# Optimization experiments

Hardware: AMD Instinct MI355X
Metric: run time of the kernel (lower is better)

The kernel has to match this reference:

```python
import jax, jax.numpy as jnp
import numpy as np

VOCAB = 8
HIDDEN = 768
DINUC_DIM = HIDDEN // 4  # 192
LN_EPS = 1e-12


def _dinuc_ids(input_ids):
    # nucleotide_map = {4:0,5:1,6:2,7:3}; dinuc id = first*4 + second if both valid else 0
    a = input_ids[:, :-1]
    b = input_ids[:, 1:]
    valid = (a >= 4) & (a <= 7) & (b >= 4) & (b <= 7)
    ids = (a - 4) * 4 + (b - 4)
    return jnp.where(valid, ids, 0)


def setup_inputs() -> dict:
    key = jax.random.key(0)
    ks = jax.random.split(key, 7)
    B, S = 32, 2048
    input_ids = jax.random.randint(ks[0], (B, S), 0, VOCAB, dtype=jnp.int64)
    token_emb = jax.random.normal(ks[1], (VOCAB, HIDDEN), dtype=jnp.float32) * 0.02
    dinuc_emb = jax.random.normal(ks[2], (16, DINUC_DIM), dtype=jnp.float32) * 0.02
    proj_W = jax.random.normal(ks[3], (HIDDEN, HIDDEN + DINUC_DIM), dtype=jnp.float32) * 0.02  # [out, in] torch layout
    proj_b = jax.random.normal(ks[4], (HIDDEN,), dtype=jnp.float32) * 0.02
    ln_gamma = jnp.ones((HIDDEN,), dtype=jnp.float32)
    ln_beta = jnp.zeros((HIDDEN,), dtype=jnp.float32)
    return {"input_ids": input_ids, "token_emb": token_emb, "dinuc_emb": dinuc_emb,
            "proj_W": proj_W, "proj_b": proj_b, "ln_gamma": ln_gamma, "ln_beta": ln_beta}


def reference(input_ids, token_emb, dinuc_emb, proj_W, proj_b, ln_gamma, ln_beta):
    # token embedding lookup: [B,S,H]
    embeddings = token_emb[input_ids]
    # dinucleotide embedding, padded with one zero row at the end: [B,S,H/4]
    d_ids = _dinuc_ids(input_ids)                      # [B,S-1]
    d_emb = dinuc_emb[d_ids]                           # [B,S-1,H/4]
    d_emb = jnp.pad(d_emb, ((0, 0), (0, 1), (0, 0)))   # [B,S,H/4]
    # concat + linear projection back to H
    concat = jnp.concatenate([embeddings, d_emb], axis=-1)  # [B,S,H+H/4]
    x = jnp.einsum('bsi,oi->bso', concat, proj_W) + proj_b
    # layernorm (eps=1e-12), dropout is identity in eval
    mu = jnp.mean(x, axis=-1, keepdims=True)
    var = jnp.mean((x - mu) ** 2, axis=-1, keepdims=True)
    return (x - mu) / jnp.sqrt(var + LN_EPS) * ln_gamma + ln_beta
```

## Files before the change

kernel.cpp:

```cpp
#include <hip/hip_runtime.h>

#define VOCAB   8
#define HIDDEN  768
#define DINUC   192
#define CONCAT  960
#define NDID    17
#define NROWS   (VOCAB * NDID)
#define SEQ     2048
#define BATCH   32
#define LN_EPS  1e-12f

__global__ void k_td(const float* __restrict__ tok,
                     const float* __restrict__ din,
                     const float* __restrict__ W,
                     float* __restrict__ TD) {
    int t = blockIdx.x * blockDim.x + threadIdx.x;
    if (t >= 24 * HIDDEN) return;
    int r = t / HIDDEN;
    int o = t - r * HIDDEN;

    float acc = 0.f;
    if (r < VOCAB) {
        const float4* e = (const float4*)(tok + r * HIDDEN);
        const float4* w = (const float4*)(W + (size_t)o * CONCAT);
        #pragma unroll 4
        for (int i = 0; i < HIDDEN / 4; ++i) {
            float4 ev = e[i], wv = w[i];
            acc += ev.x * wv.x + ev.y * wv.y + ev.z * wv.z + ev.w * wv.w;
        }
    } else {
        const float4* e = (const float4*)(din + (r - VOCAB) * DINUC);
        const float4* w = (const float4*)(W + (size_t)o * CONCAT + HIDDEN);
        #pragma unroll 4
        for (int i = 0; i < DINUC / 4; ++i) {
            float4 ev = e[i], wv = w[i];
            acc += ev.x * wv.x + ev.y * wv.y + ev.z * wv.z + ev.w * wv.w;
        }
    }
    TD[t] = acc;
}

__device__ inline float block_reduce_sum(float s, float* red) {
    int lane = threadIdx.x & 63;
    int wave = threadIdx.x >> 6;
    #pragma unroll
    for (int off = 32; off > 0; off >>= 1) s += __shfl_down(s, off, 64);
    if (lane == 0) red[wave] = s;
    __syncthreads();
    float tot = red[0] + red[1] + red[2] + red[3];
    __syncthreads();
    return tot;
}

__global__ void k_table(const float* __restrict__ TD,
                        const float* __restrict__ bias,
                        const float* __restrict__ gamma,
                        const float* __restrict__ beta,
                        float* __restrict__ table) {
    int row = blockIdx.x;
    int id  = row / NDID;
    int did = row - id * NDID;
    const float* T = TD + id * HIDDEN;
    const float* D = TD + (VOCAB + did) * HIDDEN;
    bool hasd = (did < 16);

    __shared__ float red[4];
    int tid = threadIdx.x;

    float v[3];
    float s = 0.f;
    #pragma unroll
    for (int k = 0; k < 3; ++k) {
        int o = tid + k * 256;
        float x = T[o] + bias[o];
        if (hasd) x += D[o];
        v[k] = x;
        s += x;
    }
    float mu = block_reduce_sum(s, red) * (1.f / HIDDEN);

    float sq = 0.f;
    #pragma unroll
    for (int k = 0; k < 3; ++k) {
        float d = v[k] - mu;
        sq += d * d;
    }
    float var = block_reduce_sum(sq, red) * (1.f / HIDDEN);
    float rstd = rsqrtf(var + LN_EPS);

    #pragma unroll
    for (int k = 0; k < 3; ++k) {
        int o = tid + k * 256;
        table[row * HIDDEN + o] = (v[k] - mu) * rstd * gamma[o] + beta[o];
    }
}

__global__ void k_bcast(const int* __restrict__ ids,
                        const float* __restrict__ table,
                        float4* __restrict__ out) {
    int row = blockIdx.x * 4 + threadIdx.y;
    int s   = row & (SEQ - 1);
    int a   = ids[row];
    int did;
    if (s == SEQ - 1) {
        did = 16;
    } else {
        int b = ids[row + 1];
        bool valid = (a >= 4) & (a <= 7) & (b >= 4) & (b <= 7);
        did = valid ? ((a - 4) * 4 + (b - 4)) : 0;
    }
    const float4* src = (const float4*)(table + (a * NDID + did) * HIDDEN);
    out[(size_t)row * (HIDDEN / 4) + threadIdx.x] = src[threadIdx.x];
}

extern "C" void kernel_launch(void* const* d_in, const int* in_sizes, int n_in,
                              void* d_out, int out_size, void* d_ws, size_t ws_size,
                              hipStream_t stream) {
    const int*   ids   = (const int*)d_in[0];
    const float* tok   = (const float*)d_in[1];
    const float* din   = (const float*)d_in[2];
    const float* W     = (const float*)d_in[3];
    const float* bias  = (const float*)d_in[4];
    const float* gamma = (const float*)d_in[5];
    const float* beta  = (const float*)d_in[6];

    float* table = (float*)d_ws;
    float* TD    = table + NROWS * HIDDEN;

    k_td   <<<(24 * HIDDEN + 255) / 256, 256, 0, stream>>>(tok, din, W, TD);
    k_table<<<NROWS, 256, 0, stream>>>(TD, bias, gamma, beta, table);
    k_bcast<<<(BATCH * SEQ) / 4, dim3(192, 4), 0, stream>>>(ids, table, (float4*)d_out);
}
```

Before: 265.4 us.

## Fuse projection matvec into LN table kernel and use nontemporal output stores

Drops the separate k_td kernel. Each of the 136 table-row blocks now computes the full 960-wide projection for its (token, dinuc) pair with wave-per-output dot products and shuffle reductions, then applies LayerNorm. This removes one launch and the TD round trip, but every block re-reads the whole W matrix (about 2.9 MB), so it does far more redundant work and W traffic than before. The broadcast kernel also switches to nontemporal stores for the 200 MB output to reduce cache pollution.

Measured after the change: 367.5 us. 38.4% more time.

```diff
diff --git a/kernel.cpp b/kernel.cpp
--- a/kernel.cpp
+++ b/kernel.cpp
@@ -10,74 +10,71 @@
 #define BATCH   32
 #define LN_EPS  1e-12f
 
-__global__ void k_td(const float* __restrict__ tok,
-                     const float* __restrict__ din,
-                     const float* __restrict__ W,
-                     float* __restrict__ TD) {
-    int t = blockIdx.x * blockDim.x + threadIdx.x;
-    if (t >= 24 * HIDDEN) return;
-    int r = t / HIDDEN;
-    int o = t - r * HIDDEN;
+typedef float v4f __attribute__((ext_vector_type(4)));
 
-    float acc = 0.f;
-    if (r < VOCAB) {
-        const float4* e = (const float4*)(tok + r * HIDDEN);
-        const float4* w = (const float4*)(W + (size_t)o * CONCAT);
-        #pragma unroll 4
-        for (int i = 0; i < HIDDEN / 4; ++i) {
-            float4 ev = e[i], wv = w[i];
-            acc += ev.x * wv.x + ev.y * wv.y + ev.z * wv.z + ev.w * wv.w;
-        }
-    } else {
-        const float4* e = (const float4*)(din + (r - VOCAB) * DINUC);
-        const float4* w = (const float4*)(W + (size_t)o * CONCAT + HIDDEN);
-        #pragma unroll 4
-        for (int i = 0; i < DINUC / 4; ++i) {
-            float4 ev = e[i], wv = w[i];
-            acc += ev.x * wv.x + ev.y * wv.y + ev.z * wv.z + ev.w * wv.w;
-        }
-    }
-    TD[t] = acc;
-}
-
-__device__ inline float block_reduce_sum(float s, float* red) {
-    int lane = threadIdx.x & 63;
-    int wave = threadIdx.x >> 6;
-    #pragma unroll
-    for (int off = 32; off > 0; off >>= 1) s += __shfl_down(s, off, 64);
-    if (lane == 0) red[wave] = s;
-    __syncthreads();
-    float tot = red[0] + red[1] + red[2] + red[3];
-    __syncthreads();
-    return tot;
-}
-
-__global__ void k_table(const float* __restrict__ TD,
-                        const float* __restrict__ bias,
-                        const float* __restrict__ gamma,
-                        const float* __restrict__ beta,
-                        float* __restrict__ table) {
+__global__ __launch_bounds__(256) void k_table(
+    const float* __restrict__ tok, const float* __restrict__ din,
+    const float* __restrict__ W, const float* __restrict__ bias,
+    const float* __restrict__ gamma, const float* __restrict__ beta,
+    float* __restrict__ table) {
     int row = blockIdx.x;
     int id  = row / NDID;
     int did = row - id * NDID;
-    const float* T = TD + id * HIDDEN;
-    const float* D = TD + (VOCAB + did) * HIDDEN;
-    bool hasd = (did < 16);
 
+    __shared__ float e[CONCAT];
+    __shared__ float x[HIDDEN];
     __shared__ float red[4];
+
     int tid = threadIdx.x;
+
+    for (int i = tid; i < HIDDEN; i += 256) e[i] = tok[id * HIDDEN + i];
+    if (tid < DINUC) e[HIDDEN + tid] = (did < 16) ? din[did * DINUC + tid] : 0.f;
+    __syncthreads();
+
+    int wave = tid >> 6;
+    int lane = tid & 63;
+    const float4* e4 = (const float4*)e;
+    float4 er0 = e4[lane];
+    float4 er1 = e4[64 + lane];
+    float4 er2 = e4[128 + lane];
+    float4 er3 = (lane < 48) ? e4[192 + lane] : make_float4(0.f, 0.f, 0.f, 0.f);
+
+    #pragma unroll 2
+    for (int i = 0; i < HIDDEN / 4; ++i) {
+        int o = wave * (HIDDEN / 4) + i;
+        const float4* w4 = (const float4*)(W + (size_t)o * CONCAT);
+        float4 a0 = w4[lane];
+        float4 a1 = w4[64 + lane];
+        float4 a2 = w4[128 + lane];
+        float4 a3 = (lane < 48) ? w4[192 + lane] : make_float4(0.f, 0.f, 0.f, 0.f);
+        float acc = er0.x * a0.x + er0.y * a0.y + er0.z * a0.z + er0.w * a0.w
+                  + er1.x * a1.x + er1.y * a1.y + er1.z * a1.z + er1.w * a1.w
+                  + er2.x * a2.x + er2.y * a2.y + er2.z * a2.z + er2.w * a2.w
+                  + er3.x * a3.x + er3.y * a3.y + er3.z * a3.z + er3.w * a3.w;
+        #pragma unroll
+        for (int m = 32; m; m >>= 1) acc += __shfl_xor(acc, m, 64);
+        if (lane == 0) x[o] = acc;
+    }
+    __syncthreads();
 
     float v[3];
     float s = 0.f;
     #pragma unroll
     for (int k = 0; k < 3; ++k) {
         int o = tid + k * 256;
-        float x = T[o] + bias[o];
-        if (hasd) x += D[o];
-        v[k] = x;
-        s += x;
+        float t = x[o] + bias[o];
+        v[k] = t;
+        s += t;
     }
-    float mu = block_reduce_sum(s, red) * (1.f / HIDDEN);
+    {
+        #pragma unroll
+        for (int off = 32; off; off >>= 1) s += __shfl_down(s, off, 64);
+        if (lane == 0) red[wave] = s;
+        __syncthreads();
+        s = red[0] + red[1] + red[2] + red[3];
+        __syncthreads();
+    }
+    float mu = s * (1.f / HIDDEN);
 
     float sq = 0.f;
     #pragma unroll
@@ -85,8 +82,15 @@
         float d = v[k] - mu;
         sq += d * d;
     }
-    float var = block_reduce_sum(sq, red) * (1.f / HIDDEN);
-    float rstd = rsqrtf(var + LN_EPS);
+    {
+        #pragma unroll
+        for (int off = 32; off; off >>= 1) sq += __shfl_down(sq, off, 64);
+        if (lane == 0) red[wave] = sq;
+        __syncthreads();
+        sq = red[0] + red[1] + red[2] + red[3];
+        __syncthreads();
+    }
+    float rstd = rsqrtf(sq * (1.f / HIDDEN) + LN_EPS);
 
     #pragma unroll
     for (int k = 0; k < 3; ++k) {
@@ -95,9 +99,10 @@
     }
 }
 
-__global__ void k_bcast(const int* __restrict__ ids,
-                        const float* __restrict__ table,
-                        float4* __restrict__ out) {
+__global__ __launch_bounds__(768) void k_bcast(
+    const int* __restrict__ ids,
+    const float* __restrict__ table,
+    v4f* __restrict__ out) {
     int row = blockIdx.x * 4 + threadIdx.y;
     int s   = row & (SEQ - 1);
     int a   = ids[row];
@@ -109,8 +114,9 @@
         bool valid = (a >= 4) & (a <= 7) & (b >= 4) & (b <= 7);
         did = valid ? ((a - 4) * 4 + (b - 4)) : 0;
     }
-    const float4* src = (const float4*)(table + (a * NDID + did) * HIDDEN);
-    out[(size_t)row * (HIDDEN / 4) + threadIdx.x] = src[threadIdx.x];
+    const v4f* src = (const v4f*)(table + (a * NDID + did) * HIDDEN);
+    v4f val = src[threadIdx.x];
+    __builtin_nontemporal_store(val, &out[(size_t)row * (HIDDEN / 4) + threadIdx.x]);
 }
 
 extern "C" void kernel_launch(void* const* d_in, const int* in_sizes, int n_in,
@@ -125,9 +131,7 @@
     const float* beta  = (const float*)d_in[6];
 
     float* table = (float*)d_ws;
-    float* TD    = table + NROWS * HIDDEN;
 
-    k_td   <<<(24 * HIDDEN + 255) / 256, 256, 0, stream>>>(tok, din, W, TD);
-    k_table<<<NROWS, 256, 0, stream>>>(TD, bias, gamma, beta, table);
-    k_bcast<<<(BATCH * SEQ) / 4, dim3(192, 4), 0, stream>>>(ids, table, (float4*)d_out);
+    k_table<<<NROWS, 256, 0, stream>>>(tok, din, W, bias, gamma, beta, table);
+    k_bcast<<<(BATCH * SEQ) / 4, dim3(192, 4), 0, stream>>>(ids, table, (v4f*)d_out);
 }
```

## Use wave-per-output dot products in k_td and nontemporal stores in broadcast

Applied to the files above, without the earlier changes.

The precompute kernel now assigns one 64-lane wave per output element. Lanes read contiguous float4 slices of the weight row and reduce with xor shuffles, replacing the old scheme where each thread looped serially over a full row with strided, uncoalesced weight reads. The broadcast kernel writes its roughly 200 MB output with nontemporal stores to avoid polluting the cache, and launch bounds are added to all three kernels. The main cost targeted is bandwidth on the output writes plus the serial latency of the small GEMV.

New measurement: 240.6 us. 9.4% less time.

```diff
diff --git a/kernel.cpp b/kernel.cpp
--- a/kernel.cpp
+++ b/kernel.cpp
@@ -10,41 +10,45 @@
 #define BATCH   32
 #define LN_EPS  1e-12f
 
-__global__ void k_td(const float* __restrict__ tok,
-                     const float* __restrict__ din,
-                     const float* __restrict__ W,
-                     float* __restrict__ TD) {
-    int t = blockIdx.x * blockDim.x + threadIdx.x;
-    if (t >= 24 * HIDDEN) return;
-    int r = t / HIDDEN;
-    int o = t - r * HIDDEN;
+typedef float v4f __attribute__((ext_vector_type(4)));
+
+__global__ __launch_bounds__(256) void k_td(
+    const float* __restrict__ tok, const float* __restrict__ din,
+    const float* __restrict__ W, float* __restrict__ TD) {
+    int w    = (blockIdx.x * 256 + threadIdx.x) >> 6;
+    int lane = threadIdx.x & 63;
+    int r    = w / HIDDEN;
+    int o    = w - r * HIDDEN;
 
     float acc = 0.f;
     if (r < VOCAB) {
-        const float4* e = (const float4*)(tok + r * HIDDEN);
-        const float4* w = (const float4*)(W + (size_t)o * CONCAT);
-        #pragma unroll 4
-        for (int i = 0; i < HIDDEN / 4; ++i) {
-            float4 ev = e[i], wv = w[i];
-            acc += ev.x * wv.x + ev.y * wv.y + ev.z * wv.z + ev.w * wv.w;
+        const float4* e4 = (const float4*)(tok + r * HIDDEN);
+        const float4* w4 = (const float4*)(W + (size_t)o * CONCAT);
+        #pragma unroll
+        for (int k = 0; k < 3; ++k) {
+            float4 a = w4[k * 64 + lane];
+            float4 b = e4[k * 64 + lane];
+            acc += a.x * b.x + a.y * b.y + a.z * b.z + a.w * b.w;
         }
     } else {
-        const float4* e = (const float4*)(din + (r - VOCAB) * DINUC);
-        const float4* w = (const float4*)(W + (size_t)o * CONCAT + HIDDEN);
-        #pragma unroll 4
-        for (int i = 0; i < DINUC / 4; ++i) {
-            float4 ev = e[i], wv = w[i];
-            acc += ev.x * wv.x + ev.y * wv.y + ev.z * wv.z + ev.w * wv.w;
+        if (lane < 48) {
+            const float4* e4 = (const float4*)(din + (r - VOCAB) * DINUC);
+            const float4* w4 = (const float4*)(W + (size_t)o * CONCAT + HIDDEN);
+            float4 a = w4[lane];
+            float4 b = e4[lane];
+            acc = a.x * b.x + a.y * b.y + a.z * b.z + a.w * b.w;
         }
     }
-    TD[t] = acc;
+    #pragma unroll
+    for (int m = 32; m; m >>= 1) acc += __shfl_xor(acc, m, 64);
+    if (lane == 0) TD[w] = acc;
 }
 
 __device__ inline float block_reduce_sum(float s, float* red) {
     int lane = threadIdx.x & 63;
     int wave = threadIdx.x >> 6;
     #pragma unroll
-    for (int off = 32; off > 0; off >>= 1) s += __shfl_down(s, off, 64);
+    for (int off = 32; off; off >>= 1) s += __shfl_down(s, off, 64);
     if (lane == 0) red[wave] = s;
     __syncthreads();
     float tot = red[0] + red[1] + red[2] + red[3];
@@ -52,11 +56,10 @@
     return tot;
 }
 
-__global__ void k_table(const float* __restrict__ TD,
-                        const float* __restrict__ bias,
-                        const float* __restrict__ gamma,
-                        const float* __restrict__ beta,
-                        float* __restrict__ table) {
+__global__ __launch_bounds__(256) void k_table(
+    const float* __restrict__ TD, const float* __restrict__ bias,
+    const float* __restrict__ gamma, const float* __restrict__ beta,
+    float* __restrict__ table) {
     int row = blockIdx.x;
     int id  = row / NDID;
     int did = row - id * NDID;
@@ -95,9 +98,10 @@
     }
 }
 
-__global__ void k_bcast(const int* __restrict__ ids,
-                        const float* __restrict__ table,
-                        float4* __restrict__ out) {
+__global__ __launch_bounds__(768) void k_bcast(
+    const int* __restrict__ ids,
+    const float* __restrict__ table,
+    v4f* __restrict__ out) {
     int row = blockIdx.x * 4 + threadIdx.y;
     int s   = row & (SEQ - 1);
     int a   = ids[row];
@@ -109,8 +113,9 @@
         bool valid = (a >= 4) & (a <= 7) & (b >= 4) & (b <= 7);
         did = valid ? ((a - 4) * 4 + (b - 4)) : 0;
     }
-    const float4* src = (const float4*)(table + (a * NDID + did) * HIDDEN);
-    out[(size_t)row * (HIDDEN / 4) + threadIdx.x] = src[threadIdx.x];
+    const v4f* src = (const v4f*)(table + (a * NDID + did) * HIDDEN);
+    v4f val = src[threadIdx.x];
+    __builtin_nontemporal_store(val, &out[(size_t)row * (HIDDEN / 4) + threadIdx.x]);
 }
 
 extern "C" void kernel_launch(void* const* d_in, const int* in_sizes, int n_in,
@@ -127,7 +132,7 @@
     float* table = (float*)d_ws;
     float* TD    = table + NROWS * HIDDEN;
 
-    k_td   <<<(24 * HIDDEN + 255) / 256, 256, 0, stream>>>(tok, din, W, TD);
+    k_td   <<<(24 * HIDDEN) / 4, 256, 0, stream>>>(tok, din, W, TD);
     k_table<<<NROWS, 256, 0, stream>>>(TD, bias, gamma, beta, table);
-    k_bcast<<<(BATCH * SEQ) / 4, dim3(192, 4), 0, stream>>>(ids, table, (float4*)d_out);
+    k_bcast<<<(BATCH * SEQ) / 4, dim3(192, 4), 0, stream>>>(ids, table, (v4f*)d_out);
 }
```
